# Kernel tuning notes

Hardware: AMD Instinct MI355X
Metric: run time of the kernel (lower is better)

Reference implementation:

```python
import jax, jax.numpy as jnp
import numpy as np

N_NODES = 100_000
N_EDGES = 1_600_000
N_GRAPHS = 1_000
VOCAB = 65
D_IN = 128
D_HID = 128


def setup_inputs() -> dict:
    key = jax.random.key(0)
    ks = jax.random.split(key, 12)
    x = jax.random.randint(ks[0], (N_NODES,), 0, VOCAB)
    edge_index = jax.random.randint(ks[1], (2, N_EDGES), 0, N_NODES)
    batch = jnp.sort(jax.random.randint(ks[2], (N_NODES,), 0, N_GRAPHS))

    def lin(k, fan_in, fan_out):
        bound = 1.0 / np.sqrt(fan_in)
        kw, kb = jax.random.split(k)
        W = jax.random.uniform(kw, (fan_in, fan_out), jnp.float32, -bound, bound)
        b = jax.random.uniform(kb, (fan_out,), jnp.float32, -bound, bound)
        return W, b

    emb = jax.random.normal(ks[3], (VOCAB, D_IN), jnp.float32)
    W1, b1 = lin(ks[4], D_IN, D_HID)
    W2, b2 = lin(ks[5], D_HID, D_HID)
    W3, b3 = lin(ks[6], D_HID, D_HID)
    Wf, bf = lin(ks[7], D_HID, 1)
    return {"x": x, "edge_index": edge_index, "batch": batch, "emb": emb,
            "W1": W1, "b1": b1, "W2": W2, "b2": b2, "W3": W3, "b3": b3,
            "Wf": Wf, "bf": bf}


def gcn_conv(h, W, b, src, dst, n):
    # PyG GCNConv: add self-loops, symmetric normalization D^-1/2 A_hat D^-1/2,
    # transform then aggregate messages at dst.
    h = h @ W                                             # [N, H]
    deg = jnp.zeros((n,), h.dtype).at[dst].add(1.0) + 1.0  # self-loop adds 1
    dinv = jax.lax.rsqrt(deg)                             # [N]
    coef = dinv[src] * dinv[dst]                          # [E]
    agg = jax.ops.segment_sum(h[src] * coef[:, None], dst, num_segments=n)
    return agg + h * (dinv * dinv)[:, None] + b           # self-loop term + bias


def reference(x, edge_index, batch, emb, W1, b1, W2, b2, W3, b3, Wf, bf):
    # Embedding with max_norm=1: renormalize looked-up rows to norm <= 1.
    e = emb[x]                                            # [N, D_IN]
    nrm = jnp.linalg.norm(e, axis=-1, keepdims=True)
    e = e * jnp.minimum(1.0, 1.0 / jnp.maximum(nrm, 1e-7))

    src, dst = edge_index[0], edge_index[1]
    h = jax.nn.relu(gcn_conv(e, W1, b1, src, dst, N_NODES))
    h = jax.nn.relu(gcn_conv(h, W2, b2, src, dst, N_NODES))
    h = jax.nn.relu(gcn_conv(h, W3, b3, src, dst, N_NODES))

    g = jax.ops.segment_max(h, batch, num_segments=N_GRAPHS)  # [G, H]
    return (g @ Wf + bf).ravel()                               # [G]
```

## Files before the change

### kernel.cpp

```cpp
#include <hip/hip_runtime.h>
#include <hip/hip_bf16.h>

#define N_NODES  100000
#define N_EDGES  1600000
#define N_GRAPHS 1000
#define D        128
#define CAP      64
#define NBKT     256
#define N_BUCKETS ((N_NODES + NBKT - 1) / NBKT)
#define HWGS     256
#define EPW      ((N_EDGES + HWGS - 1) / HWGS)
#define BNDB     ((N_NODES + 255) / 256)

typedef __attribute__((ext_vector_type(8))) short bf16x8;
typedef __attribute__((ext_vector_type(4))) float f32x4;

__device__ inline f32x4 mfma16(bf16x8 a, bf16x8 b, f32x4 c) {
    return __builtin_amdgcn_mfma_f32_16x16x32_bf16(a, b, c, 0, 0, 0);
}

__device__ inline unsigned short f2bf(float f) {
    unsigned u = __float_as_uint(f);
    unsigned r = u + 0x7fffu + ((u >> 16) & 1u);
    return (unsigned short)(r >> 16);
}

__global__ __launch_bounds__(256) void k_hist(const int* __restrict__ dst,
                                              int* __restrict__ bcnt,
                                              int* __restrict__ wgoff,
                                              const float* __restrict__ W1,
                                              const float* __restrict__ W2,
                                              const float* __restrict__ W3,
                                              short* __restrict__ frag,
                                              const int* __restrict__ batch,
                                              int* __restrict__ gstart,
                                              int* __restrict__ gend) {
    int w = blockIdx.x, t = threadIdx.x;
    if (w >= HWGS + 3) {
        int gid = (w - HWGS - 3) * 256 + t;
        if (gid < N_NODES) {
            int b = batch[gid];
            if (gid == 0 || batch[gid - 1] != b) gstart[b] = gid;
            if (gid == N_NODES - 1 || batch[gid + 1] != b) gend[b] = gid + 1;
        }
        return;
    }
    if (w >= HWGS) {
        int L = w - HWGS;
        const float* W = (L == 0) ? W1 : (L == 1) ? W2 : W3;
        short* fh = frag + (size_t)L * 32768;
        short* fl = fh + 16384;
        #pragma unroll
        for (int f = 0; f < 8; f++) {
            int id = t + f * 256;
            int lane = id & 63, kb = (id >> 6) & 3, nt = id >> 8;
            int k0 = kb * 32 + (lane >> 4) * 8;
            int n  = nt * 16 + (lane & 15);
            bf16x8 vh, vl;
            #pragma unroll
            for (int j = 0; j < 8; j++) {
                float wv = W[(k0 + j) * 128 + n];
                unsigned short hs = f2bf(wv);
                float hf = __uint_as_float((unsigned)hs << 16);
                vh[j] = (short)hs;
                vl[j] = (short)f2bf(wv - hf);
            }
            *(bf16x8*)&fh[id * 8] = vh;
            *(bf16x8*)&fl[id * 8] = vl;
        }
        return;
    }
    __shared__ int hist[N_BUCKETS];
    for (int b = t; b < N_BUCKETS; b += 256) hist[b] = 0;
    __syncthreads();
    int e0 = w * EPW, e1 = min(e0 + EPW, N_EDGES);
    for (int i = e0 + t; i < e1; i += 256)
        atomicAdd(&hist[dst[i] >> 8], 1);
    __syncthreads();
    for (int b = t; b < N_BUCKETS; b += 256) {
        int h = hist[b];
        wgoff[w * N_BUCKETS + b] = h ? atomicAdd(&bcnt[b], h) : 0;
    }
}

__global__ __launch_bounds__(512) void k_bscan(const int* __restrict__ bcnt,
                                               int* __restrict__ boff) {
    __shared__ int s[512];
    int t = threadIdx.x;
    int v = (t < N_BUCKETS) ? bcnt[t] : 0;
    s[t] = v;
    __syncthreads();
    for (int off = 1; off < 512; off <<= 1) {
        int val = (t >= off) ? s[t - off] : 0;
        __syncthreads();
        s[t] += val;
        __syncthreads();
    }
    if (t < N_BUCKETS) boff[t] = s[t] - v;
    if (t == 0) boff[N_BUCKETS] = N_EDGES;
}

__global__ __launch_bounds__(256) void k_scat(const int* __restrict__ src,
                                              const int* __restrict__ dst,
                                              const int* __restrict__ boff,
                                              const int* __restrict__ wgoff,
                                              int* __restrict__ ep) {
    __shared__ int cnt[N_BUCKETS];
    int t = threadIdx.x, w = blockIdx.x;
    for (int b = t; b < N_BUCKETS; b += 256) cnt[b] = 0;
    __syncthreads();
    int e0 = w * EPW, e1 = min(e0 + EPW, N_EDGES);
    for (int i = e0 + t; i < e1; i += 256) {
        int d = dst[i], b = d >> 8;
        int r = atomicAdd(&cnt[b], 1);
        ep[boff[b] + wgoff[w * N_BUCKETS + b] + r] = (src[i] << 8) | (d & 255);
    }
}

__global__ __launch_bounds__(256) void k_ell(const int* __restrict__ ep,
                                             const int* __restrict__ boff,
                                             int* __restrict__ ell,
                                             int* __restrict__ fill) {
    __shared__ int cnt_s[NBKT];
    __shared__ int ell_s[NBKT * CAP];
    int t = threadIdx.x, b = blockIdx.x;
    int nb0 = b * NBKT;
    int nn = min(NBKT, N_NODES - nb0);
    for (int i = t; i < NBKT; i += 256) cnt_s[i] = 0;
    __syncthreads();
    int e0 = boff[b], e1 = boff[b + 1];
    for (int i = e0 + t; i < e1; i += 256) {
        int e = ep[i];
        int ln = e & 255;
        int r = atomicAdd(&cnt_s[ln], 1);
        if (r < CAP) ell_s[ln * CAP + r] = (int)((unsigned)e >> 8);
    }
    __syncthreads();
    for (int i = t; i < nn * CAP; i += 256)
        ell[(size_t)nb0 * CAP + i] = ell_s[i];
    if (t < nn) fill[nb0 + t] = cnt_s[t];
}

__device__ inline void gemm_body(const short* Bh, const short* Bl,
                                 const bf16x8* a0, const bf16x8* a1,
                                 f32x4 acc[2][8], int lane) {
    #pragma unroll
    for (int kb = 0; kb < 4; kb++)
        #pragma unroll
        for (int nt = 0; nt < 8; nt++) {
            bf16x8 bh = *(const bf16x8*)&Bh[((nt * 4 + kb) * 64 + lane) * 8];
            bf16x8 bl = *(const bf16x8*)&Bl[((nt * 4 + kb) * 64 + lane) * 8];
            acc[0][nt] = mfma16(a0[kb], bh, acc[0][nt]);
            acc[0][nt] = mfma16(a0[kb], bl, acc[0][nt]);
            acc[1][nt] = mfma16(a1[kb], bh, acc[1][nt]);
            acc[1][nt] = mfma16(a1[kb], bl, acc[1][nt]);
        }
}

__device__ inline void gemm_epilogue(f32x4 acc[2][8], const int* fill,
                                     unsigned short* Cb, size_t r0,
                                     int quad, int col) {
    #pragma unroll
    for (int r = 0; r < 2; r++) {
        size_t row = r0 + r * 16 + quad * 4;
        #pragma unroll
        for (int g = 0; g < 4; g++) {
            float dv = (row + g < N_NODES)
                         ? 1.0f / sqrtf((float)fill[row + g] + 1.0f) : 0.f;
            #pragma unroll
            for (int nt = 0; nt < 8; nt++)
                Cb[(row + g) * D + nt * 16 + col] = f2bf(acc[r][nt][g] * dv);
        }
    }
}

__global__ __launch_bounds__(256) void k_gemm1e(const int* __restrict__ x,
                                                const float* __restrict__ emb,
                                                const short* __restrict__ frag,
                                                const int* __restrict__ fill,
                                                unsigned short* __restrict__ Cb) {
    __shared__ short Bfrag[2 * 16384];
    int t = threadIdx.x;
    {
        const int4* g4 = (const int4*)frag;
        int4* l4 = (int4*)Bfrag;
        #pragma unroll
        for (int i = 0; i < 16; i++) l4[t + i * 256] = g4[t + i * 256];
    }
    int w = t >> 6, lane = t & 63;
    int quad = lane >> 4, col = lane & 15;
    size_t r0 = (size_t)blockIdx.x * 128 + w * 32;

    bf16x8 a0[4], a1[4];
    {
        size_t ra = r0 + col, rb = r0 + 16 + col;
        int xa = (ra < N_NODES) ? x[ra] : 0;
        int xb = (rb < N_NODES) ? x[rb] : 0;
        float va[32], vb[32];
        float ssa = 0.f, ssb = 0.f;
        #pragma unroll
        for (int kb = 0; kb < 4; kb++) {
            float4 pa0 = *(const float4*)&emb[(size_t)xa * D + kb * 32 + quad * 8];
            float4 pa1 = *(const float4*)&emb[(size_t)xa * D + kb * 32 + quad * 8 + 4];
            float4 pb0 = *(const float4*)&emb[(size_t)xb * D + kb * 32 + quad * 8];
            float4 pb1 = *(const float4*)&emb[(size_t)xb * D + kb * 32 + quad * 8 + 4];
            va[kb*8+0]=pa0.x; va[kb*8+1]=pa0.y; va[kb*8+2]=pa0.z; va[kb*8+3]=pa0.w;
            va[kb*8+4]=pa1.x; va[kb*8+5]=pa1.y; va[kb*8+6]=pa1.z; va[kb*8+7]=pa1.w;
            vb[kb*8+0]=pb0.x; vb[kb*8+1]=pb0.y; vb[kb*8+2]=pb0.z; vb[kb*8+3]=pb0.w;
            vb[kb*8+4]=pb1.x; vb[kb*8+5]=pb1.y; vb[kb*8+6]=pb1.z; vb[kb*8+7]=pb1.w;
            #pragma unroll
            for (int j = 0; j < 8; j++) { ssa += va[kb*8+j]*va[kb*8+j];
                                          ssb += vb[kb*8+j]*vb[kb*8+j]; }
        }
        ssa += __shfl_xor(ssa, 16); ssa += __shfl_xor(ssa, 32);
        ssb += __shfl_xor(ssb, 16); ssb += __shfl_xor(ssb, 32);
        float sca = fminf(1.0f, 1.0f / fmaxf(sqrtf(ssa), 1e-7f));
        float scb = fminf(1.0f, 1.0f / fmaxf(sqrtf(ssb), 1e-7f));
        #pragma unroll
        for (int kb = 0; kb < 4; kb++) {
            bf16x8 fa, fb;
            #pragma unroll
            for (int j = 0; j < 8; j++) {
                fa[j] = (short)f2bf(va[kb*8+j] * sca);
                fb[j] = (short)f2bf(vb[kb*8+j] * scb);
            }
            a0[kb] = fa; a1[kb] = fb;
        }
    }
    f32x4 acc[2][8];
    #pragma unroll
    for (int r = 0; r < 2; r++)
        #pragma unroll
        for (int n = 0; n < 8; n++) acc[r][n] = (f32x4){0.f, 0.f, 0.f, 0.f};
    __syncthreads();
    gemm_body(Bfrag, Bfrag + 16384, a0, a1, acc, lane);
    gemm_epilogue(acc, fill, Cb, r0, quad, col);
}

__global__ __launch_bounds__(256) void k_gemm(const unsigned short* __restrict__ A,
                                              const short* __restrict__ frag,
                                              const int* __restrict__ fill,
                                              unsigned short* __restrict__ Cb) {
    __shared__ short Bfrag[2 * 16384];
    int t = threadIdx.x;
    {
        const int4* g4 = (const int4*)frag;
        int4* l4 = (int4*)Bfrag;
        #pragma unroll
        for (int i = 0; i < 16; i++) l4[t + i * 256] = g4[t + i * 256];
    }
    __syncthreads();
    int w = t >> 6, lane = t & 63;
    int quad = lane >> 4, col = lane & 15;
    size_t r0 = (size_t)blockIdx.x * 128 + w * 32;
    bf16x8 a0[4], a1[4];
    #pragma unroll
    for (int kb = 0; kb < 4; kb++) {
        a0[kb] = *(const bf16x8*)&A[(r0 + col)      * D + kb * 32 + quad * 8];
        a1[kb] = *(const bf16x8*)&A[(r0 + 16 + col) * D + kb * 32 + quad * 8];
    }
    f32x4 acc[2][8];
    #pragma unroll
    for (int r = 0; r < 2; r++)
        #pragma unroll
        for (int n = 0; n < 8; n++) acc[r][n] = (f32x4){0.f, 0.f, 0.f, 0.f};
    gemm_body(Bfrag, Bfrag + 16384, a0, a1, acc, lane);
    gemm_epilogue(acc, fill, Cb, r0, quad, col);
}

__device__ inline void acc8(float* acc, int4 r) {
    unsigned u0 = (unsigned)r.x, u1 = (unsigned)r.y,
             u2 = (unsigned)r.z, u3 = (unsigned)r.w;
    acc[0] += __uint_as_float(u0 << 16);
    acc[1] += __uint_as_float(u0 & 0xffff0000u);
    acc[2] += __uint_as_float(u1 << 16);
    acc[3] += __uint_as_float(u1 & 0xffff0000u);
    acc[4] += __uint_as_float(u2 << 16);
    acc[5] += __uint_as_float(u2 & 0xffff0000u);
    acc[6] += __uint_as_float(u3 << 16);
    acc[7] += __uint_as_float(u3 & 0xffff0000u);
}

#define LOADGRP(R, S, IT)                                                    \
    {                                                                        \
        _Pragma("unroll")                                                    \
        for (int k = 0; k < 4; k++) {                                        \
            int s = __shfl((S), (IT) * 16 + k * 4 + quad);                   \
            R[k] = *(const int4*)&hw2[((unsigned)s << 7) + cOff];            \
        }                                                                    \
    }
#define ACCGRP(A, R)                                                         \
    {                                                                        \
        _Pragma("unroll")                                                    \
        for (int k = 0; k < 4; k++) acc8((A), R[k]);                         \
    }

__global__ __launch_bounds__(256) void k_agg(const unsigned short* __restrict__ hw2,
                                             unsigned short* __restrict__ hout,
                                             const int* __restrict__ fill,
                                             const int* __restrict__ ell,
                                             const float* __restrict__ bias) {
    int w = threadIdx.x >> 6, lane = threadIdx.x & 63;
    int na = blockIdx.x * 8 + w * 2;
    int nb = na + 1;
    if (na >= N_NODES) return;
    int quad = lane >> 4;
    int l16  = lane & 15;
    unsigned cOff = (unsigned)(l16 << 3);

    int fa = __builtin_amdgcn_readfirstlane(fill[na]);
    int fb = __builtin_amdgcn_readfirstlane(fill[nb]);
    int ca = min(fa, CAP), cb = min(fb, CAP);
    int sa = (lane < ca) ? ell[na * CAP + lane] : N_NODES;
    int sb = (lane < cb) ? ell[nb * CAP + lane] : N_NODES;
    int ia = (ca + 15) >> 4; ia += (ia == 0);
    int ib = (cb + 15) >> 4; ib += (ib == 0);

    float accA[8], accB[8];
    #pragma unroll
    for (int c = 0; c < 8; c++) { accA[c] = 0.f; accB[c] = 0.f; }

    int4 A0[4], A1[4], B0[4], B1[4];
    LOADGRP(A0, sa, 0);
    LOADGRP(B0, sb, 0);
    if (1 < ia) LOADGRP(A1, sa, 1);
    ACCGRP(accA, A0);
    if (1 < ib) LOADGRP(B1, sb, 1);
    ACCGRP(accB, B0);
    if (ia > 1 || ib > 1) {
        if (2 < ia) LOADGRP(A0, sa, 2);
        if (1 < ia) ACCGRP(accA, A1);
        if (2 < ib) LOADGRP(B0, sb, 2);
        if (1 < ib) ACCGRP(accB, B1);
        if (ia > 2 || ib > 2) {
            if (3 < ia) LOADGRP(A1, sa, 3);
            if (2 < ia) ACCGRP(accA, A0);
            if (3 < ib) LOADGRP(B1, sb, 3);
            if (2 < ib) ACCGRP(accB, B0);
            if (3 < ia) ACCGRP(accA, A1);
            if (3 < ib) ACCGRP(accB, B1);
        }
    }

    #pragma unroll
    for (int c = 0; c < 8; c++) {
        accA[c] += __shfl_xor(accA[c], 16);
        accA[c] += __shfl_xor(accA[c], 32);
        accB[c] += __shfl_xor(accB[c], 16);
        accB[c] += __shfl_xor(accB[c], 32);
    }
    if (quad < 2) {
        int   n   = quad ? nb : na;
        int   fr  = quad ? fb : fa;
        float* acc = quad ? accB : accA;
        int4 sr = *(const int4*)&hw2[((unsigned)n << 7) + cOff];
        acc8(acc, sr);
        float di = 1.0f / sqrtf((float)fr + 1.0f);
        float4 bA = *(const float4*)&bias[l16 * 8];
        float4 bB = *(const float4*)&bias[l16 * 8 + 4];
        float o[8];
        o[0] = fmaxf(acc[0] * di + bA.x, 0.f);
        o[1] = fmaxf(acc[1] * di + bA.y, 0.f);
        o[2] = fmaxf(acc[2] * di + bA.z, 0.f);
        o[3] = fmaxf(acc[3] * di + bA.w, 0.f);
        o[4] = fmaxf(acc[4] * di + bB.x, 0.f);
        o[5] = fmaxf(acc[5] * di + bB.y, 0.f);
        o[6] = fmaxf(acc[6] * di + bB.z, 0.f);
        o[7] = fmaxf(acc[7] * di + bB.w, 0.f);
        int4 pk;
        pk.x = (int)((unsigned)f2bf(o[0]) | ((unsigned)f2bf(o[1]) << 16));
        pk.y = (int)((unsigned)f2bf(o[2]) | ((unsigned)f2bf(o[3]) << 16));
        pk.z = (int)((unsigned)f2bf(o[4]) | ((unsigned)f2bf(o[5]) << 16));
        pk.w = (int)((unsigned)f2bf(o[6]) | ((unsigned)f2bf(o[7]) << 16));
        *(int4*)&hout[((unsigned)n << 7) + cOff] = pk;
    }
}

__global__ __launch_bounds__(256) void k_pool(const unsigned short* __restrict__ h,
                                              const int* __restrict__ gstart,
                                              const int* __restrict__ gend,
                                              const float* __restrict__ Wf,
                                              const float* __restrict__ bf,
                                              float* __restrict__ out) {
    __shared__ float2 sm[4][64];
    int g = blockIdx.x;
    int w = threadIdx.x >> 6, lane = threadIdx.x & 63;
    int s = gstart[g], e = gend[g];
    float2 m = make_float2(-3.402823466e38f, -3.402823466e38f);
    for (int i = s + w; i < e; i += 4) {
        unsigned u = ((const unsigned*)(h + (size_t)i * D))[lane];
        m.x = fmaxf(m.x, __uint_as_float(u << 16));
        m.y = fmaxf(m.y, __uint_as_float(u & 0xffff0000u));
    }
    sm[w][lane] = m;
    __syncthreads();
    if (w == 0) {
        float2 a = sm[0][lane], b2 = sm[1][lane], c = sm[2][lane], d = sm[3][lane];
        m.x = fmaxf(fmaxf(a.x, b2.x), fmaxf(c.x, d.x));
        m.y = fmaxf(fmaxf(a.y, b2.y), fmaxf(c.y, d.y));
        float2 wf = ((const float2*)Wf)[lane];
        float val = m.x * wf.x + m.y * wf.y;
        #pragma unroll
        for (int off = 32; off; off >>= 1) val += __shfl_xor(val, off);
        if (lane == 0) out[g] = val + bf[0];
    }
}

extern "C" void kernel_launch(void* const* d_in, const int* in_sizes, int n_in,
                              void* d_out, int out_size, void* d_ws, size_t ws_size,
                              hipStream_t stream) {
    const int*   x    = (const int*)d_in[0];
    const int*   ei   = (const int*)d_in[1];
    const int*   batch= (const int*)d_in[2];
    const float* emb  = (const float*)d_in[3];
    const float* W1   = (const float*)d_in[4];
    const float* b1   = (const float*)d_in[5];
    const float* W2   = (const float*)d_in[6];
    const float* b2   = (const float*)d_in[7];
    const float* W3   = (const float*)d_in[8];
    const float* b3   = (const float*)d_in[9];
    const float* Wf   = (const float*)d_in[10];
    const float* bf   = (const float*)d_in[11];
    float* out = (float*)d_out;

    const int* src = ei;
    const int* dst = ei + N_EDGES;

    char* p = (char*)d_ws;
    unsigned short* hAb  = (unsigned short*)p; p += (size_t)(N_NODES + 128) * D * 2;
    unsigned short* hwb  = (unsigned short*)p; p += (size_t)(N_NODES + 128) * D * 2;
    int*            ep   = (int*)hwb;
    int*   fill     = (int*)p;              p += (size_t)N_NODES * 4;
    int*   gbounds  = (int*)p;              p += (size_t)2 * N_GRAPHS * 4;
    int*   ell      = (int*)p;              p += (size_t)N_NODES * CAP * 4;
    int*   wgoff    = (int*)p;              p += (size_t)HWGS * N_BUCKETS * 4;
    int*   bcnt     = (int*)p;              p += (size_t)(N_BUCKETS + 4) * 4;
    int*   boff     = (int*)p;              p += (size_t)(N_BUCKETS + 4) * 4;
    short* wfrag    = (short*)p;            p += (size_t)3 * 32768 * 2;
    (void)p;
    int* gstart = gbounds;
    int* gend   = gbounds + N_GRAPHS;

    hipMemsetAsync(bcnt, 0, (size_t)N_BUCKETS * 4, stream);
    hipMemsetAsync(gbounds, 0x7f, (size_t)2 * N_GRAPHS * 4, stream);

    const int GB = (N_NODES + 127) / 128;
    const int AB = N_NODES / 8;

    k_hist <<<HWGS + 3 + BNDB, 256, 0, stream>>>(dst, bcnt, wgoff, W1, W2, W3,
                                                 wfrag, batch, gstart, gend);
    k_bscan<<<1, 512, 0, stream>>>(bcnt, boff);
    k_scat <<<HWGS, 256, 0, stream>>>(src, dst, boff, wgoff, ep);
    k_ell  <<<N_BUCKETS, 256, 0, stream>>>(ep, boff, ell, fill);

    k_gemm1e<<<GB, 256, 0, stream>>>(x, emb, wfrag, fill, hwb);
    k_agg   <<<AB, 256, 0, stream>>>(hwb, hAb, fill, ell, b1);
    k_gemm<<<GB, 256, 0, stream>>>(hAb, wfrag + 32768, fill, hwb);
    k_agg <<<AB, 256, 0, stream>>>(hwb, hAb, fill, ell, b2);
    k_gemm<<<GB, 256, 0, stream>>>(hAb, wfrag + 65536, fill, hwb);
    k_agg <<<AB, 256, 0, stream>>>(hwb, hAb, fill, ell, b3);

    k_pool<<<N_GRAPHS, 256, 0, stream>>>(hAb, gstart, gend, Wf, bf, out);
}
```

Measured before the change: 375.8 us.

## Store node features in column-sliced layout to localize aggregation gathers

Node feature buffers move from row-major [N,128] to eight column slices of 16 bf16 each, so each slice is a compact [N,16] array. The aggregation kernel is restructured so each block handles one slice for 32 nodes, with 8 lanes per node gathering 4-byte words. The GEMM epilogue, GEMM A-loads and pooling kernel are updated to the sliced layout. The aim is to keep each slice's gather working set (about 3.2 MB) cache-resident and improve hit rates on random gathers. In exchange, gathers become narrower 4-byte accesses, and edge lists are re-read eight times, once per slice.

```diff
diff --git a/kernel.cpp b/kernel.cpp
--- a/kernel.cpp
+++ b/kernel.cpp
@@ -11,6 +11,10 @@
 #define HWGS     256
 #define EPW      ((N_EDGES + HWGS - 1) / HWGS)
 #define BNDB     ((N_NODES + 255) / 256)
+
+#define SLICE_ROWS  (N_NODES + 128)
+#define SLICE_SHORTS ((size_t)SLICE_ROWS * 16)
+#define SLICE_INTS   ((size_t)SLICE_ROWS * 8)
 
 typedef __attribute__((ext_vector_type(8))) short bf16x8;
 typedef __attribute__((ext_vector_type(4))) float f32x4;
@@ -169,7 +173,8 @@
                          ? 1.0f / sqrtf((float)fill[row + g] + 1.0f) : 0.f;
             #pragma unroll
             for (int nt = 0; nt < 8; nt++)
-                Cb[(row + g) * D + nt * 16 + col] = f2bf(acc[r][nt][g] * dv);
+                Cb[nt * SLICE_SHORTS + (row + g) * 16 + col] =
+                    f2bf(acc[r][nt][g] * dv);
         }
     }
 }
@@ -256,8 +261,10 @@
     bf16x8 a0[4], a1[4];
     #pragma unroll
     for (int kb = 0; kb < 4; kb++) {
-        a0[kb] = *(const bf16x8*)&A[(r0 + col)      * D + kb * 32 + quad * 8];
-        a1[kb] = *(const bf16x8*)&A[(r0 + 16 + col) * D + kb * 32 + quad * 8];
+        int sl  = kb * 2 + (quad >> 1);
+        int off = (quad & 1) * 8;
+        a0[kb] = *(const bf16x8*)&A[sl * SLICE_SHORTS + (r0 + col)      * 16 + off];
+        a1[kb] = *(const bf16x8*)&A[sl * SLICE_SHORTS + (r0 + 16 + col) * 16 + off];
     }
     f32x4 acc[2][8];
     #pragma unroll
@@ -267,113 +274,68 @@
     gemm_body(Bfrag, Bfrag + 16384, a0, a1, acc, lane);
     gemm_epilogue(acc, fill, Cb, r0, quad, col);
 }
-
-__device__ inline void acc8(float* acc, int4 r) {
-    unsigned u0 = (unsigned)r.x, u1 = (unsigned)r.y,
-             u2 = (unsigned)r.z, u3 = (unsigned)r.w;
-    acc[0] += __uint_as_float(u0 << 16);
-    acc[1] += __uint_as_float(u0 & 0xffff0000u);
-    acc[2] += __uint_as_float(u1 << 16);
-    acc[3] += __uint_as_float(u1 & 0xffff0000u);
-    acc[4] += __uint_as_float(u2 << 16);
-    acc[5] += __uint_as_float(u2 & 0xffff0000u);
-    acc[6] += __uint_as_float(u3 << 16);
-    acc[7] += __uint_as_float(u3 & 0xffff0000u);
-}
-
-#define LOADGRP(R, S, IT)                                                    \
-    {                                                                        \
-        _Pragma("unroll")                                                    \
-        for (int k = 0; k < 4; k++) {                                        \
-            int s = __shfl((S), (IT) * 16 + k * 4 + quad);                   \
-            R[k] = *(const int4*)&hw2[((unsigned)s << 7) + cOff];            \
-        }                                                                    \
-    }
-#define ACCGRP(A, R)                                                         \
-    {                                                                        \
-        _Pragma("unroll")                                                    \
-        for (int k = 0; k < 4; k++) acc8((A), R[k]);                         \
-    }
 
 __global__ __launch_bounds__(256) void k_agg(const unsigned short* __restrict__ hw2,
                                              unsigned short* __restrict__ hout,
                                              const int* __restrict__ fill,
                                              const int* __restrict__ ell,
                                              const float* __restrict__ bias) {
-    int w = threadIdx.x >> 6, lane = threadIdx.x & 63;
-    int na = blockIdx.x * 8 + w * 2;
-    int nb = na + 1;
-    if (na >= N_NODES) return;
-    int quad = lane >> 4;
-    int l16  = lane & 15;
-    unsigned cOff = (unsigned)(l16 << 3);
-
-    int fa = __builtin_amdgcn_readfirstlane(fill[na]);
-    int fb = __builtin_amdgcn_readfirstlane(fill[nb]);
-    int ca = min(fa, CAP), cb = min(fb, CAP);
-    int sa = (lane < ca) ? ell[na * CAP + lane] : N_NODES;
-    int sb = (lane < cb) ? ell[nb * CAP + lane] : N_NODES;
-    int ia = (ca + 15) >> 4; ia += (ia == 0);
-    int ib = (cb + 15) >> 4; ib += (ib == 0);
-
-    float accA[8], accB[8];
-    #pragma unroll
-    for (int c = 0; c < 8; c++) { accA[c] = 0.f; accB[c] = 0.f; }
-
-    int4 A0[4], A1[4], B0[4], B1[4];
-    LOADGRP(A0, sa, 0);
-    LOADGRP(B0, sb, 0);
-    if (1 < ia) LOADGRP(A1, sa, 1);
-    ACCGRP(accA, A0);
-    if (1 < ib) LOADGRP(B1, sb, 1);
-    ACCGRP(accB, B0);
-    if (ia > 1 || ib > 1) {
-        if (2 < ia) LOADGRP(A0, sa, 2);
-        if (1 < ia) ACCGRP(accA, A1);
-        if (2 < ib) LOADGRP(B0, sb, 2);
-        if (1 < ib) ACCGRP(accB, B1);
-        if (ia > 2 || ib > 2) {
-            if (3 < ia) LOADGRP(A1, sa, 3);
-            if (2 < ia) ACCGRP(accA, A0);
-            if (3 < ib) LOADGRP(B1, sb, 3);
-            if (2 < ib) ACCGRP(accB, B0);
-            if (3 < ia) ACCGRP(accA, A1);
-            if (3 < ib) ACCGRP(accB, B1);
-        }
-    }
-
-    #pragma unroll
-    for (int c = 0; c < 8; c++) {
-        accA[c] += __shfl_xor(accA[c], 16);
-        accA[c] += __shfl_xor(accA[c], 32);
-        accB[c] += __shfl_xor(accB[c], 16);
-        accB[c] += __shfl_xor(accB[c], 32);
-    }
-    if (quad < 2) {
-        int   n   = quad ? nb : na;
-        int   fr  = quad ? fb : fa;
-        float* acc = quad ? accB : accA;
-        int4 sr = *(const int4*)&hw2[((unsigned)n << 7) + cOff];
-        acc8(acc, sr);
-        float di = 1.0f / sqrtf((float)fr + 1.0f);
-        float4 bA = *(const float4*)&bias[l16 * 8];
-        float4 bB = *(const float4*)&bias[l16 * 8 + 4];
-        float o[8];
-        o[0] = fmaxf(acc[0] * di + bA.x, 0.f);
-        o[1] = fmaxf(acc[1] * di + bA.y, 0.f);
-        o[2] = fmaxf(acc[2] * di + bA.z, 0.f);
-        o[3] = fmaxf(acc[3] * di + bA.w, 0.f);
-        o[4] = fmaxf(acc[4] * di + bB.x, 0.f);
-        o[5] = fmaxf(acc[5] * di + bB.y, 0.f);
-        o[6] = fmaxf(acc[6] * di + bB.z, 0.f);
-        o[7] = fmaxf(acc[7] * di + bB.w, 0.f);
-        int4 pk;
-        pk.x = (int)((unsigned)f2bf(o[0]) | ((unsigned)f2bf(o[1]) << 16));
-        pk.y = (int)((unsigned)f2bf(o[2]) | ((unsigned)f2bf(o[3]) << 16));
-        pk.z = (int)((unsigned)f2bf(o[4]) | ((unsigned)f2bf(o[5]) << 16));
-        pk.w = (int)((unsigned)f2bf(o[6]) | ((unsigned)f2bf(o[7]) << 16));
-        *(int4*)&hout[((unsigned)n << 7) + cOff] = pk;
-    }
+    int t = threadIdx.x, w = t >> 6, lane = t & 63;
+    int s = blockIdx.x & 7;
+    int chunk = blockIdx.x >> 3;
+    int g = lane >> 3, cl = lane & 7;
+    int n = chunk * 32 + w * 8 + g;
+    const unsigned* hs = (const unsigned*)hw2 + (size_t)s * SLICE_INTS;
+
+    int fr = fill[n];
+    int cg = min(fr, CAP);
+    int base = n * CAP;
+    int sk[8];
+    #pragma unroll
+    for (int k = 0; k < 8; k++) {
+        int idx = k * 8 + cl;
+        sk[k] = (idx < cg) ? ell[base + idx] : N_NODES;
+    }
+    int cm = cg;
+    cm = max(cm, __shfl_xor(cm, 8));
+    cm = max(cm, __shfl_xor(cm, 16));
+    cm = max(cm, __shfl_xor(cm, 32));
+
+    float a0 = 0.f, a1 = 0.f;
+    int lb = lane & 0x38;
+    #pragma unroll
+    for (int k = 0; k < 8; k++) {
+        if (k * 8 < cm) {
+            #pragma unroll
+            for (int e = 0; e < 8; e += 4) {
+                int s0 = __shfl(sk[k], lb + e);
+                int s1 = __shfl(sk[k], lb + e + 1);
+                int s2 = __shfl(sk[k], lb + e + 2);
+                int s3 = __shfl(sk[k], lb + e + 3);
+                unsigned u0 = hs[(unsigned)s0 * 8 + cl];
+                unsigned u1 = hs[(unsigned)s1 * 8 + cl];
+                unsigned u2 = hs[(unsigned)s2 * 8 + cl];
+                unsigned u3 = hs[(unsigned)s3 * 8 + cl];
+                a0 += __uint_as_float(u0 << 16);
+                a1 += __uint_as_float(u0 & 0xffff0000u);
+                a0 += __uint_as_float(u1 << 16);
+                a1 += __uint_as_float(u1 & 0xffff0000u);
+                a0 += __uint_as_float(u2 << 16);
+                a1 += __uint_as_float(u2 & 0xffff0000u);
+                a0 += __uint_as_float(u3 << 16);
+                a1 += __uint_as_float(u3 & 0xffff0000u);
+            }
+        }
+    }
+    unsigned su = hs[(unsigned)n * 8 + cl];
+    a0 += __uint_as_float(su << 16);
+    a1 += __uint_as_float(su & 0xffff0000u);
+    float di = 1.0f / sqrtf((float)fr + 1.0f);
+    float2 b = *(const float2*)&bias[s * 16 + cl * 2];
+    float o0 = fmaxf(a0 * di + b.x, 0.f);
+    float o1 = fmaxf(a1 * di + b.y, 0.f);
+    unsigned pk = (unsigned)f2bf(o0) | ((unsigned)f2bf(o1) << 16);
+    ((unsigned*)hout)[(size_t)s * SLICE_INTS + (unsigned)n * 8 + cl] = pk;
 }
 
 __global__ __launch_bounds__(256) void k_pool(const unsigned short* __restrict__ h,
@@ -385,10 +347,12 @@
     __shared__ float2 sm[4][64];
     int g = blockIdx.x;
     int w = threadIdx.x >> 6, lane = threadIdx.x & 63;
+    int sl = lane >> 3, cl = lane & 7;
+    const unsigned* hp = (const unsigned*)h + (size_t)sl * SLICE_INTS;
     int s = gstart[g], e = gend[g];
     float2 m = make_float2(-3.402823466e38f, -3.402823466e38f);
     for (int i = s + w; i < e; i += 4) {
-        unsigned u = ((const unsigned*)(h + (size_t)i * D))[lane];
+        unsigned u = hp[(unsigned)i * 8 + cl];
         m.x = fmaxf(m.x, __uint_as_float(u << 16));
         m.y = fmaxf(m.y, __uint_as_float(u & 0xffff0000u));
     }
@@ -398,7 +362,7 @@
         float2 a = sm[0][lane], b2 = sm[1][lane], c = sm[2][lane], d = sm[3][lane];
         m.x = fmaxf(fmaxf(a.x, b2.x), fmaxf(c.x, d.x));
         m.y = fmaxf(fmaxf(a.y, b2.y), fmaxf(c.y, d.y));
-        float2 wf = ((const float2*)Wf)[lane];
+        float2 wf = *(const float2*)&Wf[sl * 16 + cl * 2];
         float val = m.x * wf.x + m.y * wf.y;
         #pragma unroll
         for (int off = 32; off; off >>= 1) val += __shfl_xor(val, off);
@@ -427,8 +391,8 @@
     const int* dst = ei + N_EDGES;
 
     char* p = (char*)d_ws;
-    unsigned short* hAb  = (unsigned short*)p; p += (size_t)(N_NODES + 128) * D * 2;
-    unsigned short* hwb  = (unsigned short*)p; p += (size_t)(N_NODES + 128) * D * 2;
+    unsigned short* hAb  = (unsigned short*)p; p += (size_t)SLICE_ROWS * D * 2;
+    unsigned short* hwb  = (unsigned short*)p; p += (size_t)SLICE_ROWS * D * 2;
     int*            ep   = (int*)hwb;
     int*   fill     = (int*)p;              p += (size_t)N_NODES * 4;
     int*   gbounds  = (int*)p;              p += (size_t)2 * N_GRAPHS * 4;
@@ -445,7 +409,7 @@
     hipMemsetAsync(gbounds, 0x7f, (size_t)2 * N_GRAPHS * 4, stream);
 
     const int GB = (N_NODES + 127) / 128;
-    const int AB = N_NODES / 8;
+    const int AB = (N_NODES / 32) * 8;
 
     k_hist <<<HWGS + 3 + BNDB, 256, 0, stream>>>(dst, bcnt, wgoff, W1, W2, W3,
                                                  wfrag, batch, gstart, gend);
```

Measured after the change: 427.8 us. 1.14x slower.
